# Optimization experiments

Hardware: AMD Instinct MI355X
Metric: run time of the kernel (lower is better)

The kernel has to match this reference:

```python
import jax, jax.numpy as jnp
import numpy as np

B, L, H, C, A = 8, 4096, 512, 64, 512
NEG = -1000000000.0

def setup_inputs() -> dict:
    key = jax.random.key(0)
    ks = jax.random.split(key, 6)
    hidden_states = jax.random.normal(ks[0], (B, L, H), dtype=jnp.float32)
    critical_mask = jax.random.randint(ks[1], (B, L, 1), 0, 2).astype(bool)
    count_active_channels = jax.random.randint(ks[2], (B, L, 1), 0, 64).astype(jnp.int32)
    channel_activity = jax.random.normal(ks[3], (B, L, C), dtype=jnp.float32)
    proj_w = jax.random.normal(ks[4], (H, A), dtype=jnp.float32) * 0.02
    proj_b = jnp.zeros((A,), dtype=jnp.float32)
    score_w = jax.random.normal(ks[5], (A, 1), dtype=jnp.float32) * 0.02
    score_b = jnp.zeros((1,), dtype=jnp.float32)
    return {"hidden_states": hidden_states, "critical_mask": critical_mask,
            "count_active_channels": count_active_channels,
            "channel_activity": channel_activity,
            "proj_w": proj_w, "proj_b": proj_b,
            "score_w": score_w, "score_b": score_b}

def reference(hidden_states, critical_mask, count_active_channels, channel_activity,
              proj_w, proj_b, score_w, score_b):
    mask = critical_mask[..., 0].astype(bool)                       # (B,L)
    count_signal = count_active_channels[..., 0].astype(hidden_states.dtype)  # (B,L)
    activity = jnp.maximum(channel_activity.astype(hidden_states.dtype), 0.0)  # (B,L,C)
    # score(tanh(proj(h)))  -> (B,L)
    logits = (jnp.tanh(hidden_states @ proj_w + proj_b) @ score_w + score_b)[..., 0]
    logits = logits + jnp.log1p(jnp.maximum(count_signal, 0.0))
    channel_mask = activity > 0                                      # (B,L,C)
    # (B,C,L) masked logits with log1p activity bias
    channel_logits = logits[:, None, :] + jnp.log1p(jnp.swapaxes(activity, 1, 2))
    channel_logits = jnp.where(jnp.swapaxes(channel_mask, 1, 2), channel_logits, NEG)
    has_channel_any = channel_mask.any(axis=1)                       # (B,C)
    weights = jax.nn.softmax(channel_logits, axis=-1)                # (B,C,L)
    weights = jnp.where(has_channel_any[..., None], weights, 0.0)
    channel_contexts = jnp.einsum('bcl,blh->bch', weights, hidden_states)  # (B,C,H)
    fallback = jnp.broadcast_to(hidden_states[:, -1:, :], channel_contexts.shape)
    channel_contexts = jnp.where(has_channel_any[..., None], channel_contexts, fallback)
    mix = activity / jnp.maximum(activity.sum(axis=2, keepdims=True), 1.0)  # (B,L,C)
    expanded_context = jnp.einsum('blc,bch->blh', mix, channel_contexts)    # (B,L,H)
    max_count = jnp.maximum(count_signal.max(axis=1, keepdims=True), 1.0)
    density_gate = 1.0 + count_signal / max_count                    # (B,L)
    attended = jnp.where(mask[..., None], expanded_context * density_gate[..., None], hidden_states)
    return attended, weights
```

## Files before the change

kernel.cpp:

```cpp
#include <hip/hip_runtime.h>
#include <hip/hip_bf16.h>
#include <math.h>

#define NEGV (-1000000000.0f)
constexpr int Bb = 8, Ll = 4096, Hh = 512, Cc = 64, Aa = 512;

typedef float f32x4 __attribute__((ext_vector_type(4)));
typedef short s16x8 __attribute__((ext_vector_type(8)));

__device__ inline ushort f2bf(float f) {
  union { float f; uint u; } v; v.f = f;
  uint u = v.u;
  return (ushort)((u + 0x7FFFu + ((u >> 16) & 1u)) >> 16);
}

__device__ __forceinline__ void gl16(const void* g, void* l) {
  __builtin_amdgcn_global_load_lds(
      reinterpret_cast<const __attribute__((address_space(1))) unsigned int*>(
          reinterpret_cast<uintptr_t>(g)),
      reinterpret_cast<__attribute__((address_space(3))) unsigned int*>(
          reinterpret_cast<uintptr_t>(l)),
      16, 0, 0);
}

__global__ __launch_bounds__(256) void k_front(
    const float* __restrict__ hid, const int* __restrict__ cnt,
    const float* __restrict__ sb, const float* __restrict__ pw,
    const float* __restrict__ act, ushort* __restrict__ hidb,
    ushort* __restrict__ hidbT, float* __restrict__ logits,
    ushort* __restrict__ pwT, int* __restrict__ cmax,
    float* __restrict__ actT, float* __restrict__ dinv,
    float* __restrict__ cctx) {
  __shared__ float shf[64 * 68];
  ushort* sh = (ushort*)shf;
  const int bid = blockIdx.x;
  const int tid = threadIdx.x;

  if (bid < 2048) {
    const int b = bid >> 8;
    const int rem = bid & 255;
    const int h0 = (rem >> 6) * 128;
    const int l0 = (rem & 63) * 64;
    const int rr = tid >> 5;
    const int hc4 = (tid & 31) * 4;
#pragma unroll
    for (int i = 0; i < 8; ++i) {
      int r = rr + i * 8;
      float4 f =
          *(const float4*)(hid + ((size_t)(b * Ll + l0 + r)) * Hh + h0 + hc4);
      uint u0 = (uint)f2bf(f.x) | ((uint)f2bf(f.y) << 16);
      uint u1 = (uint)f2bf(f.z) | ((uint)f2bf(f.w) << 16);
      *(uint2*)(hidb + ((size_t)(b * Ll + l0 + r)) * Hh + h0 + hc4) =
          make_uint2(u0, u1);
      *(uint2*)(sh + r * 132 + hc4) = make_uint2(u0, u1);
    }
    __syncthreads();
    const int ht = tid >> 1;
    const int d0 = (tid & 1) * 16;
    uint v[16];
#pragma unroll
    for (int k = 0; k < 16; ++k) {
      int p = d0 + k;
      v[k] = (uint)sh[(2 * p) * 132 + ht] | ((uint)sh[(2 * p + 1) * 132 + ht] << 16);
    }
    ushort* dst = hidbT + ((size_t)(b * Hh + h0 + ht)) * Ll + l0 + 2 * d0;
    *(uint4*)(dst + 0) = (uint4){v[0], v[1], v[2], v[3]};
    *(uint4*)(dst + 8) = (uint4){v[4], v[5], v[6], v[7]};
    *(uint4*)(dst + 16) = (uint4){v[8], v[9], v[10], v[11]};
    *(uint4*)(dst + 24) = (uint4){v[12], v[13], v[14], v[15]};
  } else if (bid < 2112) {
    const int bx = bid - 2048;
    const int k0 = (bx >> 3) * 64, a0 = (bx & 7) * 64;
#pragma unroll
    for (int i = 0; i < 16; ++i) {
      int e = tid + i * 256;
      int kk = e >> 6, aa = e & 63;
      sh[aa * 65 + kk] = f2bf(pw[(size_t)(k0 + kk) * Aa + a0 + aa]);
    }
    __syncthreads();
#pragma unroll
    for (int i = 0; i < 16; ++i) {
      int e = tid + i * 256;
      int aa = e >> 6, kk = e & 63;
      pwT[(size_t)(a0 + aa) * Hh + k0 + kk] = sh[aa * 65 + kk];
    }
  } else if (bid < 2240) {
    int i = (bid - 2112) * 256 + tid;
    logits[i] = sb[0] + log1pf(fmaxf((float)cnt[i], 0.f));
  } else if (bid < 2248) {
    int* shi = (int*)shf;
    const int b = bid - 2240;
    const int* p = cnt + b * Ll;
    int m = 0;
#pragma unroll
    for (int j = 0; j < 16; ++j) m = max(m, p[tid + j * 256]);
#pragma unroll
    for (int s = 32; s; s >>= 1) m = max(m, __shfl_xor(m, s));
    if ((tid & 63) == 0) shi[tid >> 6] = m;
    __syncthreads();
    if (tid == 0) cmax[b] = max(max(shi[0], shi[1]), max(shi[2], shi[3]));
  } else if (bid < 2760) {
    const int bx = bid - 2248;
    const int b = bx >> 6;
    const int l0 = (bx & 63) * 64;
    const int rr = tid >> 4;
    const int c4 = (tid & 15) * 4;
#pragma unroll
    for (int i = 0; i < 4; ++i) {
      int r = rr + i * 16;
      float4 a4 =
          *(const float4*)(act + ((size_t)(b * Ll + l0 + r)) * Cc + c4);
      a4.x = fmaxf(a4.x, 0.f);
      a4.y = fmaxf(a4.y, 0.f);
      a4.z = fmaxf(a4.z, 0.f);
      a4.w = fmaxf(a4.w, 0.f);
      *(float4*)(shf + r * 68 + c4) = a4;
    }
    __syncthreads();
    if (tid < 64) {
      float s = 0.f;
#pragma unroll 8
      for (int c = 0; c < 64; ++c) s += shf[tid * 68 + c];
      dinv[b * Ll + l0 + tid] = 1.0f / fmaxf(s, 1.0f);
    }
    const int c = tid >> 2;
    const int l16 = (tid & 3) * 16;
    float v[16];
#pragma unroll
    for (int q = 0; q < 16; ++q) v[q] = shf[(l16 + q) * 68 + c];
    float* dst = actT + ((size_t)(b * Cc + c)) * Ll + l0 + l16;
#pragma unroll
    for (int j = 0; j < 4; ++j)
      *(float4*)(dst + 4 * j) = make_float4(v[4 * j], v[4 * j + 1],
                                            v[4 * j + 2], v[4 * j + 3]);
  } else {
    const int bz = bid - 2760;
    float* p = cctx + ((size_t)(bz * 256 + tid)) * 16;
    f32x4 z = (f32x4){0.f, 0.f, 0.f, 0.f};
    *(f32x4*)(p + 0) = z;
    *(f32x4*)(p + 4) = z;
    *(f32x4*)(p + 8) = z;
    *(f32x4*)(p + 12) = z;
  }
}

__global__ __launch_bounds__(256) void k0_gemm(
    const ushort* __restrict__ hidb, const ushort* __restrict__ pwT,
    const float* __restrict__ pb, const float* __restrict__ sw,
    float* __restrict__ logits) {
  __shared__ ushort smem[16384];
  const int bm = blockIdx.x, bn = blockIdx.y;
  const int tid = threadIdx.x;
  const int lane = tid & 63;
  const int w = tid >> 6;
  const int wm = w >> 1, wn = w & 1;
  const int lc = lane & 15, lq = lane >> 4;

  const int srow = tid >> 2;
  const int schunk = (tid & 3) * 8;
  const ushort* Ag = hidb + ((size_t)(bm * 128 + srow)) * Hh + schunk;
  const ushort* Bg = pwT + ((size_t)(bn * 128 + srow)) * Hh + schunk;
  const int wrow = 16 * w;

  f32x4 acc[4][4];
#pragma unroll
  for (int mi = 0; mi < 4; ++mi)
#pragma unroll
    for (int ni = 0; ni < 4; ++ni) acc[mi][ni] = (f32x4){0.f, 0.f, 0.f, 0.f};

  const int aoffc = (wm * 64 + lc) * 32 + lq * 8;
  const int boffc = (wn * 64 + lc) * 32 + lq * 8;

#define K0_STAGE(buf, kb)                                   \
  do {                                                      \
    const ushort* ag = Ag + (kb) * 32;                      \
    const ushort* bg = Bg + (kb) * 32;                      \
    ushort* la = smem + (buf) * 4096 + wrow * 32;           \
    ushort* lb = smem + 8192 + (buf) * 4096 + wrow * 32;    \
    gl16(ag, la);                                           \
    gl16(ag + 64 * Hh, la + 64 * 32);                       \
    gl16(bg, lb);                                           \
    gl16(bg + 64 * Hh, lb + 64 * 32);                       \
  } while (0)

  K0_STAGE(0, 0);
  __syncthreads();

  int buf = 0;
  for (int kb = 0; kb < 16; ++kb) {
    if (kb < 15) K0_STAGE(buf ^ 1, kb + 1);
    const ushort* Ab = smem + buf * 4096;
    const ushort* Bt = smem + 8192 + buf * 4096;
    s16x8 af[4], bfr[4];
#pragma unroll
    for (int mi = 0; mi < 4; ++mi)
      af[mi] = *(const s16x8*)(Ab + aoffc + mi * 512);
#pragma unroll
    for (int ni = 0; ni < 4; ++ni)
      bfr[ni] = *(const s16x8*)(Bt + boffc + ni * 512);
#pragma unroll
    for (int mi = 0; mi < 4; ++mi)
#pragma unroll
      for (int ni = 0; ni < 4; ++ni)
        acc[mi][ni] = __builtin_amdgcn_mfma_f32_16x16x32_bf16(
            af[mi], bfr[ni], acc[mi][ni], 0, 0, 0);
    __syncthreads();
    buf ^= 1;
  }
#undef K0_STAGE

  float pbv[4], swv[4];
#pragma unroll
  for (int ni = 0; ni < 4; ++ni) {
    int n = bn * 128 + wn * 64 + ni * 16 + lc;
    pbv[ni] = pb[n];
    swv[ni] = sw[n];
  }
#pragma unroll
  for (int mi = 0; mi < 4; ++mi) {
#pragma unroll
    for (int r = 0; r < 4; ++r) {
      float s = 0.f;
#pragma unroll
      for (int ni = 0; ni < 4; ++ni) {
        float x = acc[mi][ni][r] + pbv[ni];
        float e = __expf(2.f * x);
        float th = 1.f - 2.f / (e + 1.f);
        s = fmaf(th, swv[ni], s);
      }
      s += __shfl_xor(s, 1);
      s += __shfl_xor(s, 2);
      s += __shfl_xor(s, 4);
      s += __shfl_xor(s, 8);
      if (lc == 0) {
        int m = bm * 128 + wm * 64 + mi * 16 + lq * 4 + r;
        atomicAdd(&logits[m], s);
      }
    }
  }
}

__global__ void k3_softmax(const float* __restrict__ actT,
                           const float* __restrict__ logits,
                           float* __restrict__ wout,
                           ushort* __restrict__ wb16,
                           int* __restrict__ hasany) {
  __shared__ float rmax[4], rcnt[4], rsum[4];
  const int bid = blockIdx.x;
  const int b = bid >> 6;
  const int tid = threadIdx.x;
  const float* arow = actT + (size_t)bid * Ll;

  float xs[16];
  float lmax = NEGV, fcnt = 0.f;
#pragma unroll
  for (int i = 0; i < 16; ++i) {
    int l = tid + i * 256;
    float a = arow[l];
    float x;
    if (a > 0.f) {
      x = logits[b * Ll + l] + log1pf(a);
      fcnt += 1.f;
    } else {
      x = NEGV;
    }
    xs[i] = x;
    lmax = fmaxf(lmax, x);
  }
#pragma unroll
  for (int m = 32; m >= 1; m >>= 1) {
    lmax = fmaxf(lmax, __shfl_xor(lmax, m));
    fcnt += __shfl_xor(fcnt, m);
  }
  if ((tid & 63) == 0) { rmax[tid >> 6] = lmax; rcnt[tid >> 6] = fcnt; }
  __syncthreads();
  float m4 = fmaxf(fmaxf(rmax[0], rmax[1]), fmaxf(rmax[2], rmax[3]));
  float call = rcnt[0] + rcnt[1] + rcnt[2] + rcnt[3];

  float lsum = 0.f;
#pragma unroll
  for (int i = 0; i < 16; ++i) {
    float e = expf(xs[i] - m4);
    xs[i] = e;
    lsum += e;
  }
#pragma unroll
  for (int m = 32; m >= 1; m >>= 1) lsum += __shfl_xor(lsum, m);
  if ((tid & 63) == 0) rsum[tid >> 6] = lsum;
  __syncthreads();
  float s = rsum[0] + rsum[1] + rsum[2] + rsum[3];
  int any = call > 0.5f;
  float inv = any ? 1.0f / s : 0.f;
#pragma unroll
  for (int i = 0; i < 16; ++i) {
    float wv = xs[i] * inv;
    wout[(size_t)bid * Ll + tid + i * 256] = wv;
    wb16[(size_t)bid * Ll + tid + i * 256] = f2bf(wv);
  }
  if (tid == 0) hasany[bid] = any;
}

__global__ __launch_bounds__(256) void k5_mfma(
    const ushort* __restrict__ wb16, const ushort* __restrict__ hidbT,
    float* __restrict__ cctx) {
  const int b = blockIdx.x, nt = blockIdx.y, kz = blockIdx.z;
  const int tid = threadIdx.x;
  const int w = tid >> 6, lane = tid & 63;
  const int lc = lane & 15, lq = lane >> 4;
  const int h0 = nt * 128 + w * 32;

  f32x4 acc[4][2];
#pragma unroll
  for (int mi = 0; mi < 4; ++mi)
#pragma unroll
    for (int ni = 0; ni < 2; ++ni) acc[mi][ni] = (f32x4){0.f, 0.f, 0.f, 0.f};

  const ushort* Abase =
      wb16 + (size_t)b * Cc * Ll + (size_t)lc * Ll + kz * 256 + lq * 8;
  const ushort* Bbase =
      hidbT + ((size_t)(b * Hh + h0 + lc)) * Ll + kz * 256 + lq * 8;

#define K5_LOAD(kb, A, Bv)                                                 \
  do {                                                                     \
    _Pragma("unroll") for (int mi = 0; mi < 4; ++mi) A[mi] =               \
        *(const s16x8*)(Abase + (size_t)mi * 16 * Ll + (kb) * 32);         \
    _Pragma("unroll") for (int ni = 0; ni < 2; ++ni) Bv[ni] =              \
        *(const s16x8*)(Bbase + (size_t)ni * 16 * Ll + (kb) * 32);         \
  } while (0)

#define K5_MFMA(A, Bv)                                                     \
  do {                                                                     \
    _Pragma("unroll") for (int mi = 0; mi < 4; ++mi)                       \
        _Pragma("unroll") for (int ni = 0; ni < 2; ++ni) acc[mi][ni] =     \
            __builtin_amdgcn_mfma_f32_16x16x32_bf16(A[mi], Bv[ni],         \
                                                    acc[mi][ni], 0, 0, 0); \
  } while (0)

  s16x8 aF[4], bF[2], aG[4], bG[2];
  K5_LOAD(0, aF, bF);
  K5_LOAD(1, aG, bG);
  K5_MFMA(aF, bF);
  K5_LOAD(2, aF, bF);
  K5_MFMA(aG, bG);
  K5_LOAD(3, aG, bG);
  K5_MFMA(aF, bF);
  K5_LOAD(4, aF, bF);
  K5_MFMA(aG, bG);
  K5_LOAD(5, aG, bG);
  K5_MFMA(aF, bF);
  K5_LOAD(6, aF, bF);
  K5_MFMA(aG, bG);
  K5_LOAD(7, aG, bG);
  K5_MFMA(aF, bF);
  K5_MFMA(aG, bG);
#undef K5_LOAD
#undef K5_MFMA

#pragma unroll
  for (int mi = 0; mi < 4; ++mi)
#pragma unroll
    for (int ni = 0; ni < 2; ++ni)
#pragma unroll
      for (int r = 0; r < 4; ++r)
        atomicAdd(&cctx[((size_t)(b * Cc + mi * 16 + lq * 4 + r)) * Hh + h0 +
                        ni * 16 + lc],
                  acc[mi][ni][r]);
}

__global__ __launch_bounds__(256) void k7_out(
    const float* __restrict__ hid, const float* __restrict__ act,
    const float* __restrict__ dinv, const float* __restrict__ cctx,
    const int* __restrict__ hasany, const int* __restrict__ mask,
    const int* __restrict__ cnt, const int* __restrict__ cmax,
    float* __restrict__ out) {
  __shared__ float cct[64][128];
  __shared__ float mixs[64][64];
  __shared__ float gateb[64];
  __shared__ int maskb[64];
  const int b = blockIdx.x;
  const int l0 = blockIdx.y * 64;
  const int h0 = blockIdx.z * 128;
  const int tid = threadIdx.x;
  const int w = tid >> 6;

  {
    const float* g = cctx + (size_t)(b * Cc + (tid >> 5)) * Hh + h0 + (tid & 31) * 4;
    float* lb = &cct[0][0] + (2 * w) * 128;
#pragma unroll
    for (int i = 0; i < 8; ++i)
      gl16(g + (size_t)(i * 8) * Hh, lb + i * 8 * 128);
  }
#pragma unroll
  for (int i = 0; i < 4; ++i) {
    int e = tid + i * 256;
    int t = e >> 4, c4 = (e & 15) * 4;
    float4 a4 = *(const float4*)(act + ((size_t)(b * Ll + l0 + t)) * Cc + c4);
    float dv = dinv[b * Ll + l0 + t];
    a4.x = fmaxf(a4.x, 0.f) * dv;
    a4.y = fmaxf(a4.y, 0.f) * dv;
    a4.z = fmaxf(a4.z, 0.f) * dv;
    a4.w = fmaxf(a4.w, 0.f) * dv;
    *(float4*)&mixs[t][c4] = a4;
  }
  if (tid < 64) {
    int l = l0 + tid;
    maskb[tid] = mask[b * Ll + l];
    gateb[tid] = 1.0f + (float)cnt[b * Ll + l] / fmaxf((float)cmax[b], 1.0f);
  }
  __syncthreads();

  {
    int c = tid >> 2, hq = (tid & 3) * 32;
    if (!hasany[b * Cc + c]) {
      const float* hl = hid + ((size_t)(b * Ll + Ll - 1)) * Hh + h0 + hq;
#pragma unroll 8
      for (int j = 0; j < 32; ++j) cct[c][hq + j] = hl[j];
    }
  }
  __syncthreads();

  const int hcol = (tid & 31) * 4;
  const int tok0 = (tid >> 5) * 8;

  f32x4 acc[8];
#pragma unroll
  for (int t = 0; t < 8; ++t) acc[t] = (f32x4){0.f, 0.f, 0.f, 0.f};

#pragma unroll 4
  for (int c0 = 0; c0 < 64; c0 += 4) {
    f32x4 cv0 = *(const f32x4*)&cct[c0 + 0][hcol];
    f32x4 cv1 = *(const f32x4*)&cct[c0 + 1][hcol];
    f32x4 cv2 = *(const f32x4*)&cct[c0 + 2][hcol];
    f32x4 cv3 = *(const f32x4*)&cct[c0 + 3][hcol];
#pragma unroll
    for (int t = 0; t < 8; ++t) {
      f32x4 mv = *(const f32x4*)&mixs[tok0 + t][c0];
      f32x4 a = acc[t];
      a = cv0 * mv.x + a;
      a = cv1 * mv.y + a;
      a = cv2 * mv.z + a;
      a = cv3 * mv.w + a;
      acc[t] = a;
    }
  }

#pragma unroll
  for (int t = 0; t < 8; ++t) {
    int tok = tok0 + t;
    size_t off = ((size_t)(b * Ll + l0 + tok)) * Hh + h0 + hcol;
    f32x4 o;
    if (maskb[tok]) {
      o = acc[t] * gateb[tok];
    } else {
      o = *(const f32x4*)(hid + off);
    }
    *(f32x4*)(out + off) = o;
  }
}

extern "C" void kernel_launch(void* const* d_in, const int* in_sizes, int n_in,
                              void* d_out, int out_size, void* d_ws,
                              size_t ws_size, hipStream_t stream) {
  const float* hid = (const float*)d_in[0];
  const int* mask = (const int*)d_in[1];
  const int* cnt = (const int*)d_in[2];
  const float* act = (const float*)d_in[3];
  const float* pw = (const float*)d_in[4];
  const float* pb = (const float*)d_in[5];
  const float* sw = (const float*)d_in[6];
  const float* sb = (const float*)d_in[7];

  float* out_att = (float*)d_out;
  float* out_w = out_att + (size_t)Bb * Ll * Hh;

  float* ws = (float*)d_ws;
  float* cctx = ws;
  int* cmaxi = (int*)(ws + 262144);
  float* logits = ws + 262152;
  float* actT = ws + 294920;
  float* dinv = ws + 2392072;
  int* hasany = (int*)(ws + 2424840);
  ushort* pwT = (ushort*)(ws + 2425352);
  ushort* wb16 = (ushort*)(ws + 2556424);

  ushort* hidb = (ushort*)out_att;
  ushort* hidbT = (ushort*)(out_att + 8388608);

  k_front<<<2824, 256, 0, stream>>>(hid, cnt, sb, pw, act, hidb, hidbT,
                                    logits, pwT, cmaxi, actT, dinv, cctx);
  k0_gemm<<<dim3(256, 4), 256, 0, stream>>>(hidb, pwT, pb, sw, logits);
  k3_softmax<<<512, 256, 0, stream>>>(actT, logits, out_w, wb16, hasany);
  k5_mfma<<<dim3(8, 4, 16), 256, 0, stream>>>(wb16, hidbT, cctx);
  k7_out<<<dim3(8, 64, 4), 256, 0, stream>>>(hid, act, dinv, cctx, hasany,
                                             mask, cnt, cmaxi, out_att);
}
```

Measured before the change: 256.8 us.

## Drop transposed bf16 hidden copy; gather B fragments from row-major hidb in k5

The front kernel no longer writes a transposed bf16 copy of hidden_states. It only converts to row-major bf16 with a simple vectorized loop. The context GEMM now builds each B fragment by gathering 8 scalar bf16 values strided by H from the row-major buffer, replacing the contiguous 16-byte loads, and the manual double-buffered load/MFMA schedule becomes a plain unrolled loop. This removes a full transposed write of the hidden tensor and the LDS transpose, at the cost of uncoalesced strided 2-byte gathers in k5 and less explicit latency hiding.

New measurement: 248.6 us. 3.2% less time.

```diff
diff --git a/kernel.cpp b/kernel.cpp
--- a/kernel.cpp
+++ b/kernel.cpp
@@ -12,6 +12,10 @@
   union { float f; uint u; } v; v.f = f;
   uint u = v.u;
   return (ushort)((u + 0x7FFFu + ((u >> 16) & 1u)) >> 16);
+}
+
+__device__ inline uint bfpack2u(float x, float y) {
+  return (uint)f2bf(x) | ((uint)f2bf(y) << 16);
 }
 
 __device__ __forceinline__ void gl16(const void* g, void* l) {
@@ -27,47 +31,24 @@
     const float* __restrict__ hid, const int* __restrict__ cnt,
     const float* __restrict__ sb, const float* __restrict__ pw,
     const float* __restrict__ act, ushort* __restrict__ hidb,
-    ushort* __restrict__ hidbT, float* __restrict__ logits,
-    ushort* __restrict__ pwT, int* __restrict__ cmax,
-    float* __restrict__ actT, float* __restrict__ dinv,
-    float* __restrict__ cctx) {
+    float* __restrict__ logits, ushort* __restrict__ pwT,
+    int* __restrict__ cmax, float* __restrict__ actT,
+    float* __restrict__ dinv, float* __restrict__ cctx) {
   __shared__ float shf[64 * 68];
   ushort* sh = (ushort*)shf;
   const int bid = blockIdx.x;
   const int tid = threadIdx.x;
 
   if (bid < 2048) {
-    const int b = bid >> 8;
-    const int rem = bid & 255;
-    const int h0 = (rem >> 6) * 128;
-    const int l0 = (rem & 63) * 64;
-    const int rr = tid >> 5;
-    const int hc4 = (tid & 31) * 4;
-#pragma unroll
-    for (int i = 0; i < 8; ++i) {
-      int r = rr + i * 8;
-      float4 f =
-          *(const float4*)(hid + ((size_t)(b * Ll + l0 + r)) * Hh + h0 + hc4);
-      uint u0 = (uint)f2bf(f.x) | ((uint)f2bf(f.y) << 16);
-      uint u1 = (uint)f2bf(f.z) | ((uint)f2bf(f.w) << 16);
-      *(uint2*)(hidb + ((size_t)(b * Ll + l0 + r)) * Hh + h0 + hc4) =
-          make_uint2(u0, u1);
-      *(uint2*)(sh + r * 132 + hc4) = make_uint2(u0, u1);
-    }
-    __syncthreads();
-    const int ht = tid >> 1;
-    const int d0 = (tid & 1) * 16;
-    uint v[16];
-#pragma unroll
-    for (int k = 0; k < 16; ++k) {
-      int p = d0 + k;
-      v[k] = (uint)sh[(2 * p) * 132 + ht] | ((uint)sh[(2 * p + 1) * 132 + ht] << 16);
-    }
-    ushort* dst = hidbT + ((size_t)(b * Hh + h0 + ht)) * Ll + l0 + 2 * d0;
-    *(uint4*)(dst + 0) = (uint4){v[0], v[1], v[2], v[3]};
-    *(uint4*)(dst + 8) = (uint4){v[4], v[5], v[6], v[7]};
-    *(uint4*)(dst + 16) = (uint4){v[8], v[9], v[10], v[11]};
-    *(uint4*)(dst + 24) = (uint4){v[12], v[13], v[14], v[15]};
+    size_t i = (size_t)bid * 256 + tid;
+#pragma unroll
+    for (int r = 0; r < 4; ++r, i += 524288) {
+      const float4* p = (const float4*)(hid + i * 8);
+      float4 x = p[0], y = p[1];
+      uint4 u = {bfpack2u(x.x, x.y), bfpack2u(x.z, x.w),
+                 bfpack2u(y.x, y.y), bfpack2u(y.z, y.w)};
+      *(uint4*)(hidb + i * 8) = u;
+    }
   } else if (bid < 2112) {
     const int bx = bid - 2048;
     const int k0 = (bx >> 3) * 64, a0 = (bx & 7) * 64;
@@ -301,7 +282,7 @@
 }
 
 __global__ __launch_bounds__(256) void k5_mfma(
-    const ushort* __restrict__ wb16, const ushort* __restrict__ hidbT,
+    const ushort* __restrict__ wb16, const ushort* __restrict__ hidb,
     float* __restrict__ cctx) {
   const int b = blockIdx.x, nt = blockIdx.y, kz = blockIdx.z;
   const int tid = threadIdx.x;
@@ -318,43 +299,30 @@
   const ushort* Abase =
       wb16 + (size_t)b * Cc * Ll + (size_t)lc * Ll + kz * 256 + lq * 8;
   const ushort* Bbase =
-      hidbT + ((size_t)(b * Hh + h0 + lc)) * Ll + kz * 256 + lq * 8;
-
-#define K5_LOAD(kb, A, Bv)                                                 \
-  do {                                                                     \
-    _Pragma("unroll") for (int mi = 0; mi < 4; ++mi) A[mi] =               \
-        *(const s16x8*)(Abase + (size_t)mi * 16 * Ll + (kb) * 32);         \
-    _Pragma("unroll") for (int ni = 0; ni < 2; ++ni) Bv[ni] =              \
-        *(const s16x8*)(Bbase + (size_t)ni * 16 * Ll + (kb) * 32);         \
-  } while (0)
-
-#define K5_MFMA(A, Bv)                                                     \
-  do {                                                                     \
-    _Pragma("unroll") for (int mi = 0; mi < 4; ++mi)                       \
-        _Pragma("unroll") for (int ni = 0; ni < 2; ++ni) acc[mi][ni] =     \
-            __builtin_amdgcn_mfma_f32_16x16x32_bf16(A[mi], Bv[ni],         \
-                                                    acc[mi][ni], 0, 0, 0); \
-  } while (0)
-
-  s16x8 aF[4], bF[2], aG[4], bG[2];
-  K5_LOAD(0, aF, bF);
-  K5_LOAD(1, aG, bG);
-  K5_MFMA(aF, bF);
-  K5_LOAD(2, aF, bF);
-  K5_MFMA(aG, bG);
-  K5_LOAD(3, aG, bG);
-  K5_MFMA(aF, bF);
-  K5_LOAD(4, aF, bF);
-  K5_MFMA(aG, bG);
-  K5_LOAD(5, aG, bG);
-  K5_MFMA(aF, bF);
-  K5_LOAD(6, aF, bF);
-  K5_MFMA(aG, bG);
-  K5_LOAD(7, aG, bG);
-  K5_MFMA(aF, bF);
-  K5_MFMA(aG, bG);
-#undef K5_LOAD
-#undef K5_MFMA
+      hidb + ((size_t)(b * Ll + kz * 256 + lq * 8)) * Hh + h0 + lc;
+
+#pragma unroll 2
+  for (int kb = 0; kb < 8; ++kb) {
+    s16x8 af[4];
+#pragma unroll
+    for (int mi = 0; mi < 4; ++mi)
+      af[mi] = *(const s16x8*)(Abase + (size_t)mi * 16 * Ll + kb * 32);
+    s16x8 bfv[2];
+#pragma unroll
+    for (int ni = 0; ni < 2; ++ni) {
+      const ushort* bp = Bbase + (size_t)kb * 32 * Hh + ni * 16;
+      s16x8 t;
+#pragma unroll
+      for (int j = 0; j < 8; ++j) t[j] = (short)bp[(size_t)j * Hh];
+      bfv[ni] = t;
+    }
+#pragma unroll
+    for (int mi = 0; mi < 4; ++mi)
+#pragma unroll
+      for (int ni = 0; ni < 2; ++ni)
+        acc[mi][ni] = __builtin_amdgcn_mfma_f32_16x16x32_bf16(
+            af[mi], bfv[ni], acc[mi][ni], 0, 0, 0);
+  }
 
 #pragma unroll
   for (int mi = 0; mi < 4; ++mi)
@@ -484,13 +452,12 @@
   ushort* wb16 = (ushort*)(ws + 2556424);
 
   ushort* hidb = (ushort*)out_att;
-  ushort* hidbT = (ushort*)(out_att + 8388608);
-
-  k_front<<<2824, 256, 0, stream>>>(hid, cnt, sb, pw, act, hidb, hidbT,
-                                    logits, pwT, cmaxi, actT, dinv, cctx);
+
+  k_front<<<2824, 256, 0, stream>>>(hid, cnt, sb, pw, act, hidb, logits, pwT,
+                                    cmaxi, actT, dinv, cctx);
   k0_gemm<<<dim3(256, 4), 256, 0, stream>>>(hidb, pwT, pb, sw, logits);
   k3_softmax<<<512, 256, 0, stream>>>(actT, logits, out_w, wb16, hasany);
-  k5_mfma<<<dim3(8, 4, 16), 256, 0, stream>>>(wb16, hidbT, cctx);
+  k5_mfma<<<dim3(8, 4, 16), 256, 0, stream>>>(wb16, hidb, cctx);
   k7_out<<<dim3(8, 64, 4), 256, 0, stream>>>(hid, act, dinv, cctx, hasany,
                                              mask, cnt, cmaxi, out_att);
 }
```
